# Kernel optimization log

Hardware: AMD Instinct MI355X
Metric: run time of the kernel (lower is better)

## Reference

```python
import jax, jax.numpy as jnp
import numpy as np

DECAY = 0.99
EPS = 1e-10
COMMIT = 0.25
K = 1024
D = 64


def setup_inputs() -> dict:
    key = jax.random.key(0)
    k1, k2, k3, k4 = jax.random.split(key, 4)
    return {
        "z_e": jax.random.normal(k1, (64, 64, 32, 32), dtype=jnp.float32),
        "embedding_w": jax.random.normal(k2, (K, D), dtype=jnp.float32),
        "ema_cluster_size": jax.random.uniform(k3, (K,), dtype=jnp.float32),
        "ema_w": jax.random.normal(k4, (K, D), dtype=jnp.float32),
    }


def reference(z_e, embedding_w, ema_cluster_size, ema_w):
    # [B, C, H, W] -> [B, H, W, C] -> [N, D]
    z_nhwc = jnp.transpose(z_e, (0, 2, 3, 1))
    z_flat = z_nhwc.reshape(-1, z_nhwc.shape[-1])

    # Squared-euclidean distances via ||z||^2 + ||e||^2 - 2 z e^T  -> [N, K]
    z_sq = jnp.sum(z_flat * z_flat, axis=1, keepdims=True)
    e_sq = jnp.sum(embedding_w * embedding_w, axis=1)
    distances = z_sq + e_sq - 2.0 * (z_flat @ embedding_w.T)

    indices = jnp.argmin(distances, axis=1)                      # [N]
    encodings = jax.nn.one_hot(indices, K, dtype=z_flat.dtype)   # [N, K]

    quantized = embedding_w[indices].reshape(z_nhwc.shape)       # [B, H, W, C]

    # --- EMA codebook update (training path; no-grad in original) ---
    counts = jnp.sum(encodings, axis=0)                          # [K]
    new_cluster_size = DECAY * ema_cluster_size + (1.0 - DECAY) * counts
    dw = encodings.T @ z_flat                                    # [K, D]
    new_ema_w = DECAY * ema_w + (1.0 - DECAY) * dw
    n = jnp.sum(new_cluster_size)
    cluster_size = (new_cluster_size + EPS) / (n + K * EPS) * n
    new_embedding_w = new_ema_w / cluster_size[:, None]

    # Commitment loss (quantized detached)
    diff = jax.lax.stop_gradient(quantized) - z_nhwc
    loss = COMMIT * jnp.mean(diff * diff)

    # Straight-through estimator
    quantized_st = z_nhwc + jax.lax.stop_gradient(quantized - z_nhwc)

    avg_probs = jnp.mean(encodings, axis=0)
    perplexity = jnp.exp(-jnp.sum(avg_probs * jnp.log(avg_probs + 1e-10)))

    quantized_out = jnp.transpose(quantized_st, (0, 3, 1, 2))    # [B, C, H, W]
    return (quantized_out, loss, perplexity, encodings,
            new_embedding_w, new_cluster_size, new_ema_w)
```

## Files before the change

### kernel.cpp

```cpp
#include <hip/hip_runtime.h>
#include <math.h>

#define NTOT 65536
#define KCB  1024
#define DIM  64

typedef float fvec2 __attribute__((ext_vector_type(2)));
typedef float fvec4 __attribute__((ext_vector_type(4)));
typedef short sh8  __attribute__((ext_vector_type(8)));

static const size_t OFF_Q    = 0;
static const size_t OFF_LOSS = 4194304;
static const size_t OFF_PERP = 4194305;
static const size_t OFF_ENC  = 4194306;
static const size_t OFF_EMB  = 71303170;
static const size_t OFF_NCS  = 71368706;
static const size_t OFF_NEMA = 71369730;

static const size_t WSO_IDX   = 0;
static const size_t WSO_ESQ   = 262144;
static const size_t WSO_LOSSP = 266240;
static const size_t WSO_CNT   = 270336;
static const size_t WSO_SCAL  = 274432;
static const size_t WSO_EBH   = 278528;
static const size_t WSO_EBL   = 409600;
static const size_t WSO_ZC    = 540672;
static const size_t WS_NEED_ZC = 540672 + (size_t)NTOT * DIM * 4;

__device__ __forceinline__ unsigned short f2bf(float f) {
    unsigned u = __builtin_bit_cast(unsigned, f);
    return (unsigned short)((u + 0x7FFFu + ((u >> 16) & 1u)) >> 16);
}
__device__ __forceinline__ float bf2f(unsigned short h) {
    unsigned u = ((unsigned)h) << 16;
    return __builtin_bit_cast(float, u);
}

__global__ void k_eprep(const float* __restrict__ emb,
                        unsigned short* __restrict__ ebh,
                        unsigned short* __restrict__ ebl,
                        float* __restrict__ esq) {
    int gid = blockIdx.x * 256 + threadIdx.x;
    int c = gid >> 3, ko8 = gid & 7;
    const fvec4* p = (const fvec4*)(emb + ((size_t)c << 6) + (ko8 << 3));
    fvec4 v0 = p[0], v1 = p[1];
    float f[8] = {v0.x, v0.y, v0.z, v0.w, v1.x, v1.y, v1.z, v1.w};
    sh8 h, l;
    float sq0 = 0.f, sq1 = 0.f;
#pragma unroll
    for (int j = 0; j < 8; ++j) {
        unsigned short hb = f2bf(f[j]);
        h[j] = (short)hb;
        l[j] = (short)f2bf(f[j] - bf2f(hb));
        if (j < 4) sq0 = fmaf(f[j], f[j], sq0); else sq1 = fmaf(f[j], f[j], sq1);
    }
    float sq = sq0 + sq1;
    sq += __shfl_xor(sq, 1, 64);
    sq += __shfl_xor(sq, 2, 64);
    sq += __shfl_xor(sq, 4, 64);
    if (ko8 == 0) esq[c] = sq;

    int ct = c >> 4, cl = c & 15, kc = ko8 >> 2, ko = ko8 & 3;
    size_t base = ((((size_t)ct << 1) + kc) << 9) + (((size_t)(ko << 4) + cl) << 3);
    *(sh8*)(ebh + base) = h;
    *(sh8*)(ebl + base) = l;
}

__global__ __launch_bounds__(256, 4)
void k_assign(const float* __restrict__ ze, const float* __restrict__ emb,
              const float* __restrict__ esq,
              const unsigned short* __restrict__ ebh,
              const unsigned short* __restrict__ ebl,
              int* __restrict__ idx_out, float* __restrict__ lossp,
              float* __restrict__ zc, int use_zc) {
    __shared__ float zt[4096];
    __shared__ float etq[4096];
    __shared__ int   sfidx[64];

    const int tid  = threadIdx.x;
    const int blk  = blockIdx.x;
    const int b    = blk >> 4;
    const int hw0  = (blk & 15) << 6;
    const int n0   = blk << 6;
    const int lane = tid & 63;
    const int wave = tid >> 6;
    const int cg   = lane & 15;
    const int ko   = lane >> 4;

#pragma unroll
    for (int j = 0; j < 4; ++j) {
        int idx = tid + (j << 8);
        int d = idx >> 4, r0 = (idx & 15) << 2;
        const fvec4 v = *(const fvec4*)(ze + (((size_t)(b << 6) + d) << 10) + hw0 + r0);
        zt[(r0 + 0) * 64 + d] = v.x;
        zt[(r0 + 1) * 64 + d] = v.y;
        zt[(r0 + 2) * 64 + d] = v.z;
        zt[(r0 + 3) * 64 + d] = v.w;
    }
    __syncthreads();

    const int arow = (wave << 4) + cg;
    sh8 Ah0, Ah1, Al0, Al1;
#pragma unroll
    for (int j = 0; j < 8; ++j) {
        float f0 = zt[arow * 64 + (ko << 3) + j];
        float f1 = zt[arow * 64 + 32 + (ko << 3) + j];
        unsigned short h0 = f2bf(f0), h1 = f2bf(f1);
        Ah0[j] = (short)h0;  Al0[j] = (short)f2bf(f0 - bf2f(h0));
        Ah1[j] = (short)h1;  Al1[j] = (short)f2bf(f1 - bf2f(h1));
    }

    float tb[4]  = {3.4e38f, 3.4e38f, 3.4e38f, 3.4e38f};
    float ts2[4] = {3.4e38f, 3.4e38f, 3.4e38f, 3.4e38f};
    int ti1[4] = {0, 0, 0, 0};
    int ti2[4] = {0, 0, 0, 0};

    const size_t lb = (size_t)lane << 3;
#define LOADB(d0, d1, d2, d3, ctv)                                  \
    { size_t o_ = ((size_t)(ctv) << 10) + lb;                       \
      d0 = *(const sh8*)(ebh + o_);                                 \
      d1 = *(const sh8*)(ebh + o_ + 512);                           \
      d2 = *(const sh8*)(ebl + o_);                                 \
      d3 = *(const sh8*)(ebl + o_ + 512); }

#define FOLD(ctv, acc)                                              \
    { const int code_ = ((ctv) << 4) + cg;                          \
      const float es_ = esq[code_];                                 \
      _Pragma("unroll")                                             \
      for (int rg = 0; rg < 4; ++rg) {                              \
          float s_ = fmaf((acc)[rg], -2.0f, es_);                   \
          bool c1 = s_ < tb[rg];                                    \
          bool c2 = s_ < ts2[rg];                                   \
          ti2[rg] = c1 ? ti1[rg] : (c2 ? code_ : ti2[rg]);          \
          ts2[rg] = c1 ? tb[rg] : (c2 ? s_ : ts2[rg]);              \
          ti1[rg] = c1 ? code_ : ti1[rg];                           \
          tb[rg]  = c1 ? s_ : tb[rg];                               \
      } }

#define TILE(i) ((((i) + (blk << 1)) & 63))

    sh8 b0h0, b0h1, b0l0, b0l1, b1h0, b1h1, b1l0, b1l1;
    LOADB(b0h0, b0h1, b0l0, b0l1, TILE(0));
    LOADB(b1h0, b1h1, b1l0, b1l1, TILE(1));

    for (int i = 0; i < 64; i += 2) {
        fvec4 aa = {0.f, 0.f, 0.f, 0.f}, ab = {0.f, 0.f, 0.f, 0.f};
        aa = __builtin_amdgcn_mfma_f32_16x16x32_bf16(Ah0, b0h0, aa, 0, 0, 0);
        ab = __builtin_amdgcn_mfma_f32_16x16x32_bf16(Ah1, b0h1, ab, 0, 0, 0);
        aa = __builtin_amdgcn_mfma_f32_16x16x32_bf16(Ah0, b0l0, aa, 0, 0, 0);
        ab = __builtin_amdgcn_mfma_f32_16x16x32_bf16(Ah1, b0l1, ab, 0, 0, 0);
        aa = __builtin_amdgcn_mfma_f32_16x16x32_bf16(Al0, b0h0, aa, 0, 0, 0);
        ab = __builtin_amdgcn_mfma_f32_16x16x32_bf16(Al1, b0h1, ab, 0, 0, 0);
        const int ct0 = TILE(i);
        if (i + 2 < 64) LOADB(b0h0, b0h1, b0l0, b0l1, TILE(i + 2));
        fvec4 acc0 = aa + ab;
        FOLD(ct0, acc0);

        fvec4 ba = {0.f, 0.f, 0.f, 0.f}, bb = {0.f, 0.f, 0.f, 0.f};
        ba = __builtin_amdgcn_mfma_f32_16x16x32_bf16(Ah0, b1h0, ba, 0, 0, 0);
        bb = __builtin_amdgcn_mfma_f32_16x16x32_bf16(Ah1, b1h1, bb, 0, 0, 0);
        ba = __builtin_amdgcn_mfma_f32_16x16x32_bf16(Ah0, b1l0, ba, 0, 0, 0);
        bb = __builtin_amdgcn_mfma_f32_16x16x32_bf16(Ah1, b1l1, bb, 0, 0, 0);
        ba = __builtin_amdgcn_mfma_f32_16x16x32_bf16(Al0, b1h0, ba, 0, 0, 0);
        bb = __builtin_amdgcn_mfma_f32_16x16x32_bf16(Al1, b1h1, bb, 0, 0, 0);
        const int ct1 = TILE(i + 1);
        if (i + 3 < 64) LOADB(b1h0, b1h1, b1l0, b1l1, TILE(i + 3));
        fvec4 acc1 = ba + bb;
        FOLD(ct1, acc1);
    }
#undef TILE
#undef LOADB
#undef FOLD

    float* mb  = etq;
    float* ms2 = etq + 1024;
    int*   mi1 = (int*)(etq + 2048);
    int*   mi2 = (int*)(etq + 3072);
#pragma unroll
    for (int rg = 0; rg < 4; ++rg) {
        int row = (wave << 4) + (ko << 2) + rg;
        mb [(cg << 6) + row] = tb[rg];
        ms2[(cg << 6) + row] = ts2[rg];
        mi1[(cg << 6) + row] = ti1[rg];
        mi2[(cg << 6) + row] = ti2[rg];
    }
    __syncthreads();

    if (tid < 64) {
        const int r = tid;
        float fb = mb[r], fs2 = ms2[r];
        int fi1 = mi1[r], fi2 = mi2[r];
#pragma unroll
        for (int p = 1; p < 16; ++p) {
            float ob = mb[(p << 6) + r], os2 = ms2[(p << 6) + r];
            int oi1 = mi1[(p << 6) + r], oi2 = mi2[(p << 6) + r];
            if (ob < fb)       { fs2 = fb; fi2 = fi1; fb = ob; fi1 = oi1; }
            else if (ob < fs2) { fs2 = ob; fi2 = oi1; }
            if (os2 < fs2)     { fs2 = os2; fi2 = oi2; }
        }
        if (fs2 - fb < 2e-2f) {
            double d1 = 0.0, d2 = 0.0;
            const float* e1 = emb + (size_t)fi1 * 64;
            const float* e2 = emb + (size_t)fi2 * 64;
            for (int d = 0; d < 64; ++d) {
                double zd = (double)zt[r * 64 + d];
                double q1 = zd - (double)e1[d];
                double q2 = zd - (double)e2[d];
                d1 += q1 * q1;
                d2 += q2 * q2;
            }
            if ((d2 < d1) || (d2 == d1 && fi2 < fi1)) fi1 = fi2;
        }
        sfidx[r] = fi1;
        idx_out[n0 + r] = fi1;
    }
    __syncthreads();

    float lacc = 0.f;
    for (int i = tid; i < 1024; i += 256) {
        int r = i >> 4, d4 = (i & 15) << 2;
        const fvec4 zv = *(const fvec4*)&zt[(r << 6) + d4];
        const fvec4 ev = *(const fvec4*)(emb + ((size_t)sfidx[r] << 6) + d4);
        fvec4 df = ev - zv;
        lacc = fmaf(df.x, df.x, lacc);
        lacc = fmaf(df.y, df.y, lacc);
        lacc = fmaf(df.z, df.z, lacc);
        lacc = fmaf(df.w, df.w, lacc);
        if (use_zc)
            *(fvec4*)&zc[(((size_t)(n0 + r)) << 6) + d4] = zv;
    }
    __syncthreads();

    float* lred = etq;
    lred[tid] = lacc;
    __syncthreads();
    for (int s = 128; s > 0; s >>= 1) {
        if (tid < s) lred[tid] += lred[tid + s];
        __syncthreads();
    }
    if (tid == 0) lossp[blk] = lred[0];
}

__global__ __launch_bounds__(256)
void k_tail(const int* __restrict__ idx, const float* __restrict__ zcmp,
            const float* __restrict__ ze, const float* __restrict__ emaw,
            const float* __restrict__ ecs, const float* __restrict__ emb,
            float* __restrict__ out, int* __restrict__ counts, int use_zc) {
    __shared__ __align__(16) char smem[17424];
    const int t = threadIdx.x;

    if (blockIdx.x & 1) {
        const int blk = blockIdx.x >> 1;
        const int b   = blk >> 4;
        const int hw0 = (blk & 15) << 6;
        const int n0  = blk << 6;
        int*   sfidx = (int*)smem;
        float* qt    = (float*)(smem + 256);

        if (t < 64) sfidx[t] = idx[n0 + t];
        __syncthreads();

        for (int i = t; i < 4096; i += 256) {
            int r = i >> 6, d = i & 63;
            qt[d * 65 + r] = emb[(size_t)sfidx[r] * 64 + d];
        }

        float* ebase = out + OFF_ENC;
        if (t < 255) {
            const int cb = 2 + (t << 2);
            for (int r = 0; r < 64; ++r) {
                const int fi = sfidx[r];
                fvec4 v;
                v.x = (fi == cb)     ? 1.0f : 0.0f;
                v.y = (fi == cb + 1) ? 1.0f : 0.0f;
                v.z = (fi == cb + 2) ? 1.0f : 0.0f;
                v.w = (fi == cb + 3) ? 1.0f : 0.0f;
                __builtin_nontemporal_store(
                    v, (fvec4*)(ebase + ((size_t)(n0 + r) << 10) + cb));
            }
        } else {
            for (int r = 0; r < 64; ++r) {
                const int fi = sfidx[r];
                float* rowp = ebase + ((size_t)(n0 + r) << 10);
                fvec2 hd, tl;
                hd.x = (fi == 0)    ? 1.0f : 0.0f;
                hd.y = (fi == 1)    ? 1.0f : 0.0f;
                tl.x = (fi == 1022) ? 1.0f : 0.0f;
                tl.y = (fi == 1023) ? 1.0f : 0.0f;
                __builtin_nontemporal_store(hd, (fvec2*)rowp);
                __builtin_nontemporal_store(tl, (fvec2*)(rowp + 1022));
            }
        }
        __syncthreads();

        for (int i = t; i < 4096; i += 256) {
            int d = i >> 6, r = i & 63;
            __builtin_nontemporal_store(
                qt[d * 65 + r],
                &out[OFF_Q + ((size_t)((b << 6) + d) << 10) + hw0 + r]);
        }
        return;
    }

    const int k    = blockIdx.x >> 1;
    const int g    = t >> 6;
    const int d    = t & 63;
    const int lane = t & 63;
    int*   s_list = (int*)smem;
    int*   s_wsum = (int*)(smem + 16384);
    float* s_red  = (float*)(smem + 16400);

#define ZLOAD(n) (use_zc ? zcmp[((size_t)(n) << 6) + d] \
                         : ze[((((size_t)((n) >> 10) << 6) + d) << 10) + ((n) & 1023)])

    float a0 = 0.f, a1 = 0.f, a2 = 0.f, a3 = 0.f;
    int totalM = 0;

    for (int chunk = 0; chunk < 16; ++chunk) {
        const int base = chunk << 12;
        const int nb   = base + (t << 4);
        const int4* ip = (const int4*)(idx + nb);
        const int4 v0 = ip[0], v1 = ip[1], v2 = ip[2], v3 = ip[3];

        int c = 0;
        c += (v0.x == k) + (v0.y == k) + (v0.z == k) + (v0.w == k);
        c += (v1.x == k) + (v1.y == k) + (v1.z == k) + (v1.w == k);
        c += (v2.x == k) + (v2.y == k) + (v2.z == k) + (v2.w == k);
        c += (v3.x == k) + (v3.y == k) + (v3.z == k) + (v3.w == k);

        int inc = c;
#pragma unroll
        for (int off = 1; off < 64; off <<= 1) {
            int y = __shfl_up(inc, (unsigned)off, 64);
            if (lane >= off) inc += y;
        }
        if (lane == 63) s_wsum[g] = inc;
        __syncthreads();

        int wbase = 0;
#pragma unroll
        for (int w = 0; w < 4; ++w) wbase += (w < g) ? s_wsum[w] : 0;
        const int M = s_wsum[0] + s_wsum[1] + s_wsum[2] + s_wsum[3];
        int pos = wbase + inc - c;

        if (v0.x == k) s_list[pos++] = nb + 0;
        if (v0.y == k) s_list[pos++] = nb + 1;
        if (v0.z == k) s_list[pos++] = nb + 2;
        if (v0.w == k) s_list[pos++] = nb + 3;
        if (v1.x == k) s_list[pos++] = nb + 4;
        if (v1.y == k) s_list[pos++] = nb + 5;
        if (v1.z == k) s_list[pos++] = nb + 6;
        if (v1.w == k) s_list[pos++] = nb + 7;
        if (v2.x == k) s_list[pos++] = nb + 8;
        if (v2.y == k) s_list[pos++] = nb + 9;
        if (v2.z == k) s_list[pos++] = nb + 10;
        if (v2.w == k) s_list[pos++] = nb + 11;
        if (v3.x == k) s_list[pos++] = nb + 12;
        if (v3.y == k) s_list[pos++] = nb + 13;
        if (v3.z == k) s_list[pos++] = nb + 14;
        if (v3.w == k) s_list[pos++] = nb + 15;
        __syncthreads();

        int j = g;
        for (; j + 12 < M; j += 16) {
            int n0_ = s_list[j], n1_ = s_list[j + 4];
            int n2_ = s_list[j + 8], n3_ = s_list[j + 12];
            float z0 = ZLOAD(n0_), z1 = ZLOAD(n1_);
            float z2 = ZLOAD(n2_), z3 = ZLOAD(n3_);
            a0 += z0; a1 += z1; a2 += z2; a3 += z3;
        }
        for (; j < M; j += 4) a0 += ZLOAD(s_list[j]);
        totalM += M;
        __syncthreads();
    }
#undef ZLOAD

    s_red[(g << 6) + d] = (a0 + a1) + (a2 + a3);
    __syncthreads();
    if (g == 0) {
        float s = ((s_red[d] + s_red[64 + d]) + s_red[128 + d]) + s_red[192 + d];
        out[OFF_NEMA + ((size_t)k << 6) + d] =
            fmaf(0.01f, s, 0.99f * emaw[((size_t)k << 6) + d]);
    }
    if (t == 0) {
        counts[k] = totalM;
        out[OFF_NCS + k] = fmaf(0.01f, (float)totalM, 0.99f * ecs[k]);
    }
}

__global__ void k_scalars(const float* __restrict__ lossp, const int* __restrict__ counts,
                          const float* __restrict__ ncs, float* __restrict__ out,
                          float* __restrict__ scal) {
    __shared__ float sr[256];
    const int t = threadIdx.x;

    float v = lossp[t] + lossp[t + 256] + lossp[t + 512] + lossp[t + 768];
    sr[t] = v;
    __syncthreads();
    for (int s = 128; s > 0; s >>= 1) { if (t < s) sr[t] += sr[t + s]; __syncthreads(); }
    if (t == 0) out[OFF_LOSS] = sr[0] * (0.25f / 4194304.0f);
    __syncthreads();

    v = ncs[t] + ncs[t + 256] + ncs[t + 512] + ncs[t + 768];
    sr[t] = v;
    __syncthreads();
    for (int s = 128; s > 0; s >>= 1) { if (t < s) sr[t] += sr[t + s]; __syncthreads(); }
    if (t == 0) scal[0] = sr[0];
    __syncthreads();

    float pv = 0.f;
    for (int i = t; i < 1024; i += 256) {
        float p = (float)counts[i] * (1.0f / 65536.0f);
        pv += p * logf(p + 1e-10f);
    }
    sr[t] = pv;
    __syncthreads();
    for (int s = 128; s > 0; s >>= 1) { if (t < s) sr[t] += sr[t + s]; __syncthreads(); }
    if (t == 0) out[OFF_PERP] = expf(-sr[0]);
}

__global__ void k_embnorm(const float* __restrict__ nema, const float* __restrict__ ncs,
                          const float* __restrict__ scal, float* __restrict__ embw) {
    int i = blockIdx.x * 256 + threadIdx.x;
    float n = scal[0];
    int k = i >> 6;
    float cs = (ncs[k] + 1e-10f) / (n + 1.024e-7f) * n;
    embw[i] = nema[i] / cs;
}

extern "C" void kernel_launch(void* const* d_in, const int* in_sizes, int n_in,
                              void* d_out, int out_size, void* d_ws, size_t ws_size,
                              hipStream_t stream) {
    const float* ze   = (const float*)d_in[0];
    const float* emb  = (const float*)d_in[1];
    const float* ecs  = (const float*)d_in[2];
    const float* emaw = (const float*)d_in[3];
    float* out = (float*)d_out;
    char*  ws  = (char*)d_ws;

    int*            idx    = (int*)(ws + WSO_IDX);
    float*          esq    = (float*)(ws + WSO_ESQ);
    float*          lossp  = (float*)(ws + WSO_LOSSP);
    int*            counts = (int*)(ws + WSO_CNT);
    float*          scal   = (float*)(ws + WSO_SCAL);
    unsigned short* ebh    = (unsigned short*)(ws + WSO_EBH);
    unsigned short* ebl    = (unsigned short*)(ws + WSO_EBL);
    float*          zc     = (float*)(ws + WSO_ZC);
    const int use_zc = (ws_size >= WS_NEED_ZC) ? 1 : 0;

    k_eprep  <<<32,   256, 0, stream>>>(emb, ebh, ebl, esq);
    k_assign <<<1024, 256, 0, stream>>>(ze, emb, esq, ebh, ebl, idx, lossp, zc, use_zc);
    k_tail   <<<2048, 256, 0, stream>>>(idx, zc, ze, emaw, ecs, emb, out, counts, use_zc);
    k_scalars<<<1,    256, 0, stream>>>(lossp, counts, out + OFF_NCS, out, scal);
    k_embnorm<<<256,  256, 0, stream>>>(out + OFF_NEMA, out + OFF_NCS, scal, out + OFF_EMB);
}
```

Measured before the change: 153.2 us.

## Stage codebook tiles through a double-buffered LDS ring shared by the block

Previously each of the four waves loaded every bf16 hi/lo codebook tile straight from global memory into registers, so each tile was fetched four times per block. Now the block loads each tile cooperatively, one 16-byte load per thread, and stores it into a two-slot LDS buffer; every wave then reads its MFMA operands from LDS. The esq norms are also copied into LDS once per block. The cost is a __syncthreads per tile, 64 per block, and shorter per-wave prefetch distance, which can stall the small 6-MFMA loop body.

After: 164.6 us. +7.4%, slower.

```diff
diff --git a/kernel.cpp b/kernel.cpp
--- a/kernel.cpp
+++ b/kernel.cpp
@@ -74,7 +74,7 @@
               int* __restrict__ idx_out, float* __restrict__ lossp,
               float* __restrict__ zc, int use_zc) {
     __shared__ float zt[4096];
-    __shared__ float etq[4096];
+    __shared__ __align__(16) float etq[4096];
     __shared__ int   sfidx[64];
 
     const int tid  = threadIdx.x;
@@ -87,6 +87,10 @@
     const int cg   = lane & 15;
     const int ko   = lane >> 4;
 
+    char*  ebuf0 = (char*)etq;
+    char*  ebuf1 = (char*)etq + 4096;
+    float* esql  = etq + 2048;
+
 #pragma unroll
     for (int j = 0; j < 4; ++j) {
         int idx = tid + (j << 8);
@@ -97,6 +101,19 @@
         zt[(r0 + 2) * 64 + d] = v.z;
         zt[(r0 + 3) * 64 + d] = v.w;
     }
+    {
+        fvec4 e4 = *(const fvec4*)(esq + (tid << 2));
+        *(fvec4*)&esql[tid << 2] = e4;
+    }
+
+    const unsigned short* sgbase = (tid < 128) ? ebh : ebl;
+    const int soff   = (tid & 127) << 3;
+    const int dstoff = (tid < 128) ? (tid << 4) : (2048 + ((tid - 128) << 4));
+    const size_t lo  = (size_t)lane << 4;
+
+#define TILE(i) ((((i) + (blk << 1)) & 63))
+
+    sh8 stg = *(const sh8*)(sgbase + ((size_t)TILE(0) << 10) + soff);
     __syncthreads();
 
     const int arow = (wave << 4) + cg;
@@ -110,67 +127,52 @@
         Ah1[j] = (short)h1;  Al1[j] = (short)f2bf(f1 - bf2f(h1));
     }
 
+    *(sh8*)(ebuf0 + dstoff) = stg;
+    __syncthreads();
+
     float tb[4]  = {3.4e38f, 3.4e38f, 3.4e38f, 3.4e38f};
     float ts2[4] = {3.4e38f, 3.4e38f, 3.4e38f, 3.4e38f};
     int ti1[4] = {0, 0, 0, 0};
     int ti2[4] = {0, 0, 0, 0};
 
-    const size_t lb = (size_t)lane << 3;
-#define LOADB(d0, d1, d2, d3, ctv)                                  \
-    { size_t o_ = ((size_t)(ctv) << 10) + lb;                       \
-      d0 = *(const sh8*)(ebh + o_);                                 \
-      d1 = *(const sh8*)(ebh + o_ + 512);                           \
-      d2 = *(const sh8*)(ebl + o_);                                 \
-      d3 = *(const sh8*)(ebl + o_ + 512); }
-
-#define FOLD(ctv, acc)                                              \
-    { const int code_ = ((ctv) << 4) + cg;                          \
-      const float es_ = esq[code_];                                 \
-      _Pragma("unroll")                                             \
-      for (int rg = 0; rg < 4; ++rg) {                              \
-          float s_ = fmaf((acc)[rg], -2.0f, es_);                   \
-          bool c1 = s_ < tb[rg];                                    \
-          bool c2 = s_ < ts2[rg];                                   \
-          ti2[rg] = c1 ? ti1[rg] : (c2 ? code_ : ti2[rg]);          \
-          ts2[rg] = c1 ? tb[rg] : (c2 ? s_ : ts2[rg]);              \
-          ti1[rg] = c1 ? code_ : ti1[rg];                           \
-          tb[rg]  = c1 ? s_ : tb[rg];                               \
-      } }
-
-#define TILE(i) ((((i) + (blk << 1)) & 63))
-
-    sh8 b0h0, b0h1, b0l0, b0l1, b1h0, b1h1, b1l0, b1l1;
-    LOADB(b0h0, b0h1, b0l0, b0l1, TILE(0));
-    LOADB(b1h0, b1h1, b1l0, b1l1, TILE(1));
-
-    for (int i = 0; i < 64; i += 2) {
+    for (int i = 0; i < 64; ++i) {
+        const int ct = TILE(i);
+        const char* rb = (i & 1) ? ebuf1 : ebuf0;
+        char*       wb = (i & 1) ? ebuf0 : ebuf1;
+        if (i < 63)
+            stg = *(const sh8*)(sgbase + ((size_t)TILE(i + 1) << 10) + soff);
+
+        sh8 bh0 = *(const sh8*)(rb + lo);
+        sh8 bh1 = *(const sh8*)(rb + 1024 + lo);
+        sh8 bl0 = *(const sh8*)(rb + 2048 + lo);
+        sh8 bl1 = *(const sh8*)(rb + 3072 + lo);
+
         fvec4 aa = {0.f, 0.f, 0.f, 0.f}, ab = {0.f, 0.f, 0.f, 0.f};
-        aa = __builtin_amdgcn_mfma_f32_16x16x32_bf16(Ah0, b0h0, aa, 0, 0, 0);
-        ab = __builtin_amdgcn_mfma_f32_16x16x32_bf16(Ah1, b0h1, ab, 0, 0, 0);
-        aa = __builtin_amdgcn_mfma_f32_16x16x32_bf16(Ah0, b0l0, aa, 0, 0, 0);
-        ab = __builtin_amdgcn_mfma_f32_16x16x32_bf16(Ah1, b0l1, ab, 0, 0, 0);
-        aa = __builtin_amdgcn_mfma_f32_16x16x32_bf16(Al0, b0h0, aa, 0, 0, 0);
-        ab = __builtin_amdgcn_mfma_f32_16x16x32_bf16(Al1, b0h1, ab, 0, 0, 0);
-        const int ct0 = TILE(i);
-        if (i + 2 < 64) LOADB(b0h0, b0h1, b0l0, b0l1, TILE(i + 2));
-        fvec4 acc0 = aa + ab;
-        FOLD(ct0, acc0);
-
-        fvec4 ba = {0.f, 0.f, 0.f, 0.f}, bb = {0.f, 0.f, 0.f, 0.f};
-        ba = __builtin_amdgcn_mfma_f32_16x16x32_bf16(Ah0, b1h0, ba, 0, 0, 0);
-        bb = __builtin_amdgcn_mfma_f32_16x16x32_bf16(Ah1, b1h1, bb, 0, 0, 0);
-        ba = __builtin_amdgcn_mfma_f32_16x16x32_bf16(Ah0, b1l0, ba, 0, 0, 0);
-        bb = __builtin_amdgcn_mfma_f32_16x16x32_bf16(Ah1, b1l1, bb, 0, 0, 0);
-        ba = __builtin_amdgcn_mfma_f32_16x16x32_bf16(Al0, b1h0, ba, 0, 0, 0);
-        bb = __builtin_amdgcn_mfma_f32_16x16x32_bf16(Al1, b1h1, bb, 0, 0, 0);
-        const int ct1 = TILE(i + 1);
-        if (i + 3 < 64) LOADB(b1h0, b1h1, b1l0, b1l1, TILE(i + 3));
-        fvec4 acc1 = ba + bb;
-        FOLD(ct1, acc1);
+        aa = __builtin_amdgcn_mfma_f32_16x16x32_bf16(Ah0, bh0, aa, 0, 0, 0);
+        ab = __builtin_amdgcn_mfma_f32_16x16x32_bf16(Ah1, bh1, ab, 0, 0, 0);
+        aa = __builtin_amdgcn_mfma_f32_16x16x32_bf16(Ah0, bl0, aa, 0, 0, 0);
+        ab = __builtin_amdgcn_mfma_f32_16x16x32_bf16(Ah1, bl1, ab, 0, 0, 0);
+        aa = __builtin_amdgcn_mfma_f32_16x16x32_bf16(Al0, bh0, aa, 0, 0, 0);
+        ab = __builtin_amdgcn_mfma_f32_16x16x32_bf16(Al1, bh1, ab, 0, 0, 0);
+        fvec4 acc = aa + ab;
+
+        const int code = (ct << 4) + cg;
+        const float es = esql[code];
+#pragma unroll
+        for (int rg = 0; rg < 4; ++rg) {
+            float s = fmaf(acc[rg], -2.0f, es);
+            bool c1 = s < tb[rg];
+            bool c2 = s < ts2[rg];
+            ti2[rg] = c1 ? ti1[rg] : (c2 ? code : ti2[rg]);
+            ts2[rg] = c1 ? tb[rg] : (c2 ? s : ts2[rg]);
+            ti1[rg] = c1 ? code : ti1[rg];
+            tb[rg]  = c1 ? s : tb[rg];
+        }
+
+        if (i < 63) *(sh8*)(wb + dstoff) = stg;
+        __syncthreads();
     }
 #undef TILE
-#undef LOADB
-#undef FOLD
 
     float* mb  = etq;
     float* ms2 = etq + 1024;
```

## Fuse one-hot and quantized output writes into assign kernel; prefetch esq

Applied to the files above, without the earlier changes.

Moves the one-hot encoding stores and the transposed quantized-output writes from the tail kernel into the assignment kernel. The gathered codebook rows already in registers are staged through a swizzled shared-memory tile, which avoids re-reading indices and embeddings in a separate pass. The tail kernel becomes a stats-only kernel with half the blocks. It also software-prefetches the esq value alongside the B-tile loads. The trade-off is a longer assign kernel, so the large 268MB encoding write is no longer overlapped with the stats blocks in the same launch.

New measurement: 187.4 us. 1.22x slower.

```diff
diff --git a/kernel.cpp b/kernel.cpp
--- a/kernel.cpp
+++ b/kernel.cpp
@@ -34,6 +34,10 @@
 __device__ __forceinline__ float bf2f(unsigned short h) {
     unsigned u = ((unsigned)h) << 16;
     return __builtin_bit_cast(float, u);
+}
+
+__device__ __forceinline__ int swz(int r, int d) {
+    return (r << 6) + ((((d >> 2) ^ ((r >> 2) & 15)) << 2) | (d & 3));
 }
 
 __global__ void k_eprep(const float* __restrict__ emb,
@@ -71,10 +75,11 @@
               const float* __restrict__ esq,
               const unsigned short* __restrict__ ebh,
               const unsigned short* __restrict__ ebl,
+              float* __restrict__ out,
               int* __restrict__ idx_out, float* __restrict__ lossp,
               float* __restrict__ zc, int use_zc) {
     __shared__ float zt[4096];
-    __shared__ float etq[4096];
+    __shared__ __align__(16) float etq[4096];
     __shared__ int   sfidx[64];
 
     const int tid  = threadIdx.x;
@@ -123,12 +128,11 @@
       d2 = *(const sh8*)(ebl + o_);                                 \
       d3 = *(const sh8*)(ebl + o_ + 512); }
 
-#define FOLD(ctv, acc)                                              \
+#define FOLD(ctv, acc, esv)                                         \
     { const int code_ = ((ctv) << 4) + cg;                          \
-      const float es_ = esq[code_];                                 \
       _Pragma("unroll")                                             \
       for (int rg = 0; rg < 4; ++rg) {                              \
-          float s_ = fmaf((acc)[rg], -2.0f, es_);                   \
+          float s_ = fmaf((acc)[rg], -2.0f, (esv));                 \
           bool c1 = s_ < tb[rg];                                    \
           bool c2 = s_ < ts2[rg];                                   \
           ti2[rg] = c1 ? ti1[rg] : (c2 ? code_ : ti2[rg]);          \
@@ -142,6 +146,8 @@
     sh8 b0h0, b0h1, b0l0, b0l1, b1h0, b1h1, b1l0, b1l1;
     LOADB(b0h0, b0h1, b0l0, b0l1, TILE(0));
     LOADB(b1h0, b1h1, b1l0, b1l1, TILE(1));
+    float es0 = esq[(TILE(0) << 4) + cg];
+    float es1 = esq[(TILE(1) << 4) + cg];
 
     for (int i = 0; i < 64; i += 2) {
         fvec4 aa = {0.f, 0.f, 0.f, 0.f}, ab = {0.f, 0.f, 0.f, 0.f};
@@ -152,9 +158,13 @@
         aa = __builtin_amdgcn_mfma_f32_16x16x32_bf16(Al0, b0h0, aa, 0, 0, 0);
         ab = __builtin_amdgcn_mfma_f32_16x16x32_bf16(Al1, b0h1, ab, 0, 0, 0);
         const int ct0 = TILE(i);
-        if (i + 2 < 64) LOADB(b0h0, b0h1, b0l0, b0l1, TILE(i + 2));
+        const float esc0 = es0;
+        if (i + 2 < 64) {
+            LOADB(b0h0, b0h1, b0l0, b0l1, TILE(i + 2));
+            es0 = esq[(TILE(i + 2) << 4) + cg];
+        }
         fvec4 acc0 = aa + ab;
-        FOLD(ct0, acc0);
+        FOLD(ct0, acc0, esc0);
 
         fvec4 ba = {0.f, 0.f, 0.f, 0.f}, bb = {0.f, 0.f, 0.f, 0.f};
         ba = __builtin_amdgcn_mfma_f32_16x16x32_bf16(Ah0, b1h0, ba, 0, 0, 0);
@@ -164,9 +174,13 @@
         ba = __builtin_amdgcn_mfma_f32_16x16x32_bf16(Al0, b1h0, ba, 0, 0, 0);
         bb = __builtin_amdgcn_mfma_f32_16x16x32_bf16(Al1, b1h1, bb, 0, 0, 0);
         const int ct1 = TILE(i + 1);
-        if (i + 3 < 64) LOADB(b1h0, b1h1, b1l0, b1l1, TILE(i + 3));
+        const float esc1 = es1;
+        if (i + 3 < 64) {
+            LOADB(b1h0, b1h1, b1l0, b1l1, TILE(i + 3));
+            es1 = esq[(TILE(i + 3) << 4) + cg];
+        }
         fvec4 acc1 = ba + bb;
-        FOLD(ct1, acc1);
+        FOLD(ct1, acc1, esc1);
     }
 #undef TILE
 #undef LOADB
@@ -226,8 +240,47 @@
         lacc = fmaf(df.y, df.y, lacc);
         lacc = fmaf(df.z, df.z, lacc);
         lacc = fmaf(df.w, df.w, lacc);
+        etq[swz(d4 + 0, r)] = ev.x;
+        etq[swz(d4 + 1, r)] = ev.y;
+        etq[swz(d4 + 2, r)] = ev.z;
+        etq[swz(d4 + 3, r)] = ev.w;
         if (use_zc)
             *(fvec4*)&zc[(((size_t)(n0 + r)) << 6) + d4] = zv;
+    }
+
+    float* ebase = out + OFF_ENC;
+    if (tid < 255) {
+        const int cb = 2 + (tid << 2);
+        for (int r = 0; r < 64; ++r) {
+            const int fi = sfidx[r];
+            fvec4 v;
+            v.x = (fi == cb)     ? 1.0f : 0.0f;
+            v.y = (fi == cb + 1) ? 1.0f : 0.0f;
+            v.z = (fi == cb + 2) ? 1.0f : 0.0f;
+            v.w = (fi == cb + 3) ? 1.0f : 0.0f;
+            __builtin_nontemporal_store(
+                v, (fvec4*)(ebase + ((size_t)(n0 + r) << 10) + cb));
+        }
+    } else {
+        for (int r = 0; r < 64; ++r) {
+            const int fi = sfidx[r];
+            float* rowp = ebase + ((size_t)(n0 + r) << 10);
+            fvec2 hd, tl;
+            hd.x = (fi == 0)    ? 1.0f : 0.0f;
+            hd.y = (fi == 1)    ? 1.0f : 0.0f;
+            tl.x = (fi == 1022) ? 1.0f : 0.0f;
+            tl.y = (fi == 1023) ? 1.0f : 0.0f;
+            __builtin_nontemporal_store(hd, (fvec2*)rowp);
+            __builtin_nontemporal_store(tl, (fvec2*)(rowp + 1022));
+        }
+    }
+    __syncthreads();
+
+    for (int i = tid; i < 4096; i += 256) {
+        int d = i >> 6, r = i & 63;
+        __builtin_nontemporal_store(
+            etq[swz(d, r)],
+            &out[OFF_Q + ((size_t)((b << 6) + d) << 10) + hw0 + r]);
     }
     __syncthreads();
 
@@ -242,73 +295,19 @@
 }
 
 __global__ __launch_bounds__(256)
-void k_tail(const int* __restrict__ idx, const float* __restrict__ zcmp,
-            const float* __restrict__ ze, const float* __restrict__ emaw,
-            const float* __restrict__ ecs, const float* __restrict__ emb,
-            float* __restrict__ out, int* __restrict__ counts, int use_zc) {
-    __shared__ __align__(16) char smem[17424];
-    const int t = threadIdx.x;
-
-    if (blockIdx.x & 1) {
-        const int blk = blockIdx.x >> 1;
-        const int b   = blk >> 4;
-        const int hw0 = (blk & 15) << 6;
-        const int n0  = blk << 6;
-        int*   sfidx = (int*)smem;
-        float* qt    = (float*)(smem + 256);
-
-        if (t < 64) sfidx[t] = idx[n0 + t];
-        __syncthreads();
-
-        for (int i = t; i < 4096; i += 256) {
-            int r = i >> 6, d = i & 63;
-            qt[d * 65 + r] = emb[(size_t)sfidx[r] * 64 + d];
-        }
-
-        float* ebase = out + OFF_ENC;
-        if (t < 255) {
-            const int cb = 2 + (t << 2);
-            for (int r = 0; r < 64; ++r) {
-                const int fi = sfidx[r];
-                fvec4 v;
-                v.x = (fi == cb)     ? 1.0f : 0.0f;
-                v.y = (fi == cb + 1) ? 1.0f : 0.0f;
-                v.z = (fi == cb + 2) ? 1.0f : 0.0f;
-                v.w = (fi == cb + 3) ? 1.0f : 0.0f;
-                __builtin_nontemporal_store(
-                    v, (fvec4*)(ebase + ((size_t)(n0 + r) << 10) + cb));
-            }
-        } else {
-            for (int r = 0; r < 64; ++r) {
-                const int fi = sfidx[r];
-                float* rowp = ebase + ((size_t)(n0 + r) << 10);
-                fvec2 hd, tl;
-                hd.x = (fi == 0)    ? 1.0f : 0.0f;
-                hd.y = (fi == 1)    ? 1.0f : 0.0f;
-                tl.x = (fi == 1022) ? 1.0f : 0.0f;
-                tl.y = (fi == 1023) ? 1.0f : 0.0f;
-                __builtin_nontemporal_store(hd, (fvec2*)rowp);
-                __builtin_nontemporal_store(tl, (fvec2*)(rowp + 1022));
-            }
-        }
-        __syncthreads();
-
-        for (int i = t; i < 4096; i += 256) {
-            int d = i >> 6, r = i & 63;
-            __builtin_nontemporal_store(
-                qt[d * 65 + r],
-                &out[OFF_Q + ((size_t)((b << 6) + d) << 10) + hw0 + r]);
-        }
-        return;
-    }
-
-    const int k    = blockIdx.x >> 1;
+void k_stats(const int* __restrict__ idx, const float* __restrict__ zcmp,
+             const float* __restrict__ ze, const float* __restrict__ emaw,
+             const float* __restrict__ ecs, float* __restrict__ out,
+             int* __restrict__ counts, int use_zc) {
+    const int k    = blockIdx.x;
+    const int t    = threadIdx.x;
     const int g    = t >> 6;
     const int d    = t & 63;
     const int lane = t & 63;
-    int*   s_list = (int*)smem;
-    int*   s_wsum = (int*)(smem + 16384);
-    float* s_red  = (float*)(smem + 16400);
+
+    __shared__ int   s_list[4096];
+    __shared__ int   s_wsum[4];
+    __shared__ float s_red[4][64];
 
 #define ZLOAD(n) (use_zc ? zcmp[((size_t)(n) << 6) + d] \
                          : ze[((((size_t)((n) >> 10) << 6) + d) << 10) + ((n) & 1023)])
@@ -375,10 +374,10 @@
     }
 #undef ZLOAD
 
-    s_red[(g << 6) + d] = (a0 + a1) + (a2 + a3);
+    s_red[g][d] = (a0 + a1) + (a2 + a3);
     __syncthreads();
     if (g == 0) {
-        float s = ((s_red[d] + s_red[64 + d]) + s_red[128 + d]) + s_red[192 + d];
+        float s = ((s_red[0][d] + s_red[1][d]) + s_red[2][d]) + s_red[3][d];
         out[OFF_NEMA + ((size_t)k << 6) + d] =
             fmaf(0.01f, s, 0.99f * emaw[((size_t)k << 6) + d]);
     }
@@ -449,8 +448,8 @@
     const int use_zc = (ws_size >= WS_NEED_ZC) ? 1 : 0;
 
     k_eprep  <<<32,   256, 0, stream>>>(emb, ebh, ebl, esq);
-    k_assign <<<1024, 256, 0, stream>>>(ze, emb, esq, ebh, ebl, idx, lossp, zc, use_zc);
-    k_tail   <<<2048, 256, 0, stream>>>(idx, zc, ze, emaw, ecs, emb, out, counts, use_zc);
+    k_assign <<<1024, 256, 0, stream>>>(ze, emb, esq, ebh, ebl, out, idx, lossp, zc, use_zc);
+    k_stats  <<<1024, 256, 0, stream>>>(idx, zc, ze, emaw, ecs, out, counts, use_zc);
     k_scalars<<<1,    256, 0, stream>>>(lossp, counts, out + OFF_NCS, out, scal);
     k_embnorm<<<256,  256, 0, stream>>>(out + OFF_NEMA, out + OFF_NCS, scal, out + OFF_EMB);
 }
```

## Split codebook scatter into 16-code by 4096-row tiles with separate reduction kernel

Applied to the files above, without the earlier changes.

Before, each k_tail block owned one code and scanned all 65536 indices across 16 chunks. Now each block owns 16 codes and a 4096-row slice. It accumulates per-code partial sums in shared memory, tallies counts with LDS atomics, and writes partials to workspace. A new k_red kernel sums the 16 slices and applies the EMA update. The aim is to cut the redundant index scanning by 16x, at the cost of an extra launch, about 4MB of partial traffic, and a larger shared-memory footprint per block.

Measured after the change: 155.1 us. No clear change (+1.3%).

```diff
diff --git a/kernel.cpp b/kernel.cpp
--- a/kernel.cpp
+++ b/kernel.cpp
@@ -24,8 +24,10 @@
 static const size_t WSO_SCAL  = 274432;
 static const size_t WSO_EBH   = 278528;
 static const size_t WSO_EBL   = 409600;
-static const size_t WSO_ZC    = 540672;
-static const size_t WS_NEED_ZC = 540672 + (size_t)NTOT * DIM * 4;
+static const size_t WSO_PDW   = 540672;
+static const size_t WSO_PCNT  = 4734976;
+static const size_t WSO_ZC    = 4800512;
+static const size_t WS_NEED_ZC = 4800512 + (size_t)NTOT * DIM * 4;
 
 __device__ __forceinline__ unsigned short f2bf(float f) {
     unsigned u = __builtin_bit_cast(unsigned, f);
@@ -243,10 +245,10 @@
 
 __global__ __launch_bounds__(256)
 void k_tail(const int* __restrict__ idx, const float* __restrict__ zcmp,
-            const float* __restrict__ ze, const float* __restrict__ emaw,
-            const float* __restrict__ ecs, const float* __restrict__ emb,
-            float* __restrict__ out, int* __restrict__ counts, int use_zc) {
-    __shared__ __align__(16) char smem[17424];
+            const float* __restrict__ ze, const float* __restrict__ emb,
+            float* __restrict__ out, float* __restrict__ pdw,
+            int* __restrict__ pcnt, int use_zc) {
+    __shared__ __align__(16) char smem[32864];
     const int t = threadIdx.x;
 
     if (blockIdx.x & 1) {
@@ -302,89 +304,104 @@
         return;
     }
 
-    const int k    = blockIdx.x >> 1;
+    const int sidx = blockIdx.x >> 1;
+    const int kg   = sidx & 63;
+    const int ng   = sidx >> 6;
+    const int k0   = kg << 4;
     const int g    = t >> 6;
     const int d    = t & 63;
     const int lane = t & 63;
+
     int*   s_list = (int*)smem;
-    int*   s_wsum = (int*)(smem + 16384);
-    float* s_red  = (float*)(smem + 16400);
-
-#define ZLOAD(n) (use_zc ? zcmp[((size_t)(n) << 6) + d] \
-                         : ze[((((size_t)((n) >> 10) << 6) + d) << 10) + ((n) & 1023)])
-
-    float a0 = 0.f, a1 = 0.f, a2 = 0.f, a3 = 0.f;
-    int totalM = 0;
-
-    for (int chunk = 0; chunk < 16; ++chunk) {
-        const int base = chunk << 12;
-        const int nb   = base + (t << 4);
-        const int4* ip = (const int4*)(idx + nb);
-        const int4 v0 = ip[0], v1 = ip[1], v2 = ip[2], v3 = ip[3];
-
+    float* part   = (float*)(smem + 16384);
+    int*   s_wsum = (int*)(smem + 32768);
+    int*   s_cnt  = (int*)(smem + 32784);
+
+    for (int i = t; i < 4096; i += 256) part[i] = 0.f;
+    if (t < 16) s_cnt[t] = 0;
+
+    const int nb = (ng << 12) + (t << 4);
+    const int4* ip = (const int4*)(idx + nb);
+    const int4 v0 = ip[0], v1 = ip[1], v2 = ip[2], v3 = ip[3];
+
+#define MM(x) ((unsigned)((x) - k0) < 16u)
+    int c = 0;
+    c += MM(v0.x) + MM(v0.y) + MM(v0.z) + MM(v0.w);
+    c += MM(v1.x) + MM(v1.y) + MM(v1.z) + MM(v1.w);
+    c += MM(v2.x) + MM(v2.y) + MM(v2.z) + MM(v2.w);
+    c += MM(v3.x) + MM(v3.y) + MM(v3.z) + MM(v3.w);
+
+    int inc = c;
+#pragma unroll
+    for (int off = 1; off < 64; off <<= 1) {
+        int y = __shfl_up(inc, (unsigned)off, 64);
+        if (lane >= off) inc += y;
+    }
+    if (lane == 63) s_wsum[g] = inc;
+    __syncthreads();
+
+    int wbase = 0;
+#pragma unroll
+    for (int w = 0; w < 4; ++w) wbase += (w < g) ? s_wsum[w] : 0;
+    const int M = s_wsum[0] + s_wsum[1] + s_wsum[2] + s_wsum[3];
+    int pos = wbase + inc - c;
+
+#define EMIT(x, o) if (MM(x)) { s_list[pos++] = (((t << 4) + (o)) << 4) | ((x) - k0); \
+                                atomicAdd(&s_cnt[(x) - k0], 1); }
+    EMIT(v0.x, 0)  EMIT(v0.y, 1)  EMIT(v0.z, 2)  EMIT(v0.w, 3)
+    EMIT(v1.x, 4)  EMIT(v1.y, 5)  EMIT(v1.z, 6)  EMIT(v1.w, 7)
+    EMIT(v2.x, 8)  EMIT(v2.y, 9)  EMIT(v2.z, 10) EMIT(v2.w, 11)
+    EMIT(v3.x, 12) EMIT(v3.y, 13) EMIT(v3.z, 14) EMIT(v3.w, 15)
+#undef EMIT
+#undef MM
+    __syncthreads();
+
+#define ZL(nloc) (use_zc ? zcmp[(((size_t)((ng << 12) + (nloc))) << 6) + d] \
+                         : ze[((((size_t)(((ng << 12) + (nloc)) >> 10) << 6) + d) << 10) + (((ng << 12) + (nloc)) & 1023)])
+    {
+        float* pg = part + (g << 10);
+        int j = g;
+        for (; j + 4 < M; j += 8) {
+            int e0 = s_list[j], e1 = s_list[j + 4];
+            float f0 = ZL(e0 >> 4);
+            float f1 = ZL(e1 >> 4);
+            pg[((e0 & 15) << 6) + d] += f0;
+            pg[((e1 & 15) << 6) + d] += f1;
+        }
+        for (; j < M; j += 4) {
+            int e0 = s_list[j];
+            pg[((e0 & 15) << 6) + d] += ZL(e0 >> 4);
+        }
+    }
+#undef ZL
+    __syncthreads();
+
+    for (int i = t; i < 1024; i += 256) {
+        float s = ((part[i] + part[1024 + i]) + part[2048 + i]) + part[3072 + i];
+        int cc = i >> 6, dd = i & 63;
+        pdw[(((size_t)(ng << 10) + k0 + cc) << 6) + dd] = s;
+    }
+    if (t < 16) pcnt[(ng << 10) + k0 + t] = s_cnt[t];
+}
+
+__global__ __launch_bounds__(256)
+void k_red(const float* __restrict__ pdw, const int* __restrict__ pcnt,
+           const float* __restrict__ emaw, const float* __restrict__ ecs,
+           float* __restrict__ out, int* __restrict__ counts) {
+    const int gid = blockIdx.x * 256 + threadIdx.x;
+    const int k = gid >> 6, d = gid & 63;
+    float s = 0.f;
+#pragma unroll
+    for (int ng = 0; ng < 16; ++ng)
+        s += pdw[(((size_t)(ng << 10) + k) << 6) + d];
+    out[OFF_NEMA + ((size_t)k << 6) + d] =
+        fmaf(0.01f, s, 0.99f * emaw[((size_t)k << 6) + d]);
+    if (d == 0) {
         int c = 0;
-        c += (v0.x == k) + (v0.y == k) + (v0.z == k) + (v0.w == k);
-        c += (v1.x == k) + (v1.y == k) + (v1.z == k) + (v1.w == k);
-        c += (v2.x == k) + (v2.y == k) + (v2.z == k) + (v2.w == k);
-        c += (v3.x == k) + (v3.y == k) + (v3.z == k) + (v3.w == k);
-
-        int inc = c;
-#pragma unroll
-        for (int off = 1; off < 64; off <<= 1) {
-            int y = __shfl_up(inc, (unsigned)off, 64);
-            if (lane >= off) inc += y;
-        }
-        if (lane == 63) s_wsum[g] = inc;
-        __syncthreads();
-
-        int wbase = 0;
-#pragma unroll
-        for (int w = 0; w < 4; ++w) wbase += (w < g) ? s_wsum[w] : 0;
-        const int M = s_wsum[0] + s_wsum[1] + s_wsum[2] + s_wsum[3];
-        int pos = wbase + inc - c;
-
-        if (v0.x == k) s_list[pos++] = nb + 0;
-        if (v0.y == k) s_list[pos++] = nb + 1;
-        if (v0.z == k) s_list[pos++] = nb + 2;
-        if (v0.w == k) s_list[pos++] = nb + 3;
-        if (v1.x == k) s_list[pos++] = nb + 4;
-        if (v1.y == k) s_list[pos++] = nb + 5;
-        if (v1.z == k) s_list[pos++] = nb + 6;
-        if (v1.w == k) s_list[pos++] = nb + 7;
-        if (v2.x == k) s_list[pos++] = nb + 8;
-        if (v2.y == k) s_list[pos++] = nb + 9;
-        if (v2.z == k) s_list[pos++] = nb + 10;
-        if (v2.w == k) s_list[pos++] = nb + 11;
-        if (v3.x == k) s_list[pos++] = nb + 12;
-        if (v3.y == k) s_list[pos++] = nb + 13;
-        if (v3.z == k) s_list[pos++] = nb + 14;
-        if (v3.w == k) s_list[pos++] = nb + 15;
-        __syncthreads();
-
-        int j = g;
-        for (; j + 12 < M; j += 16) {
-            int n0_ = s_list[j], n1_ = s_list[j + 4];
-            int n2_ = s_list[j + 8], n3_ = s_list[j + 12];
-            float z0 = ZLOAD(n0_), z1 = ZLOAD(n1_);
-            float z2 = ZLOAD(n2_), z3 = ZLOAD(n3_);
-            a0 += z0; a1 += z1; a2 += z2; a3 += z3;
-        }
-        for (; j < M; j += 4) a0 += ZLOAD(s_list[j]);
-        totalM += M;
-        __syncthreads();
-    }
-#undef ZLOAD
-
-    s_red[(g << 6) + d] = (a0 + a1) + (a2 + a3);
-    __syncthreads();
-    if (g == 0) {
-        float s = ((s_red[d] + s_red[64 + d]) + s_red[128 + d]) + s_red[192 + d];
-        out[OFF_NEMA + ((size_t)k << 6) + d] =
-            fmaf(0.01f, s, 0.99f * emaw[((size_t)k << 6) + d]);
-    }
-    if (t == 0) {
-        counts[k] = totalM;
-        out[OFF_NCS + k] = fmaf(0.01f, (float)totalM, 0.99f * ecs[k]);
+#pragma unroll
+        for (int ng = 0; ng < 16; ++ng) c += pcnt[(ng << 10) + k];
+        counts[k] = c;
+        out[OFF_NCS + k] = fmaf(0.01f, (float)c, 0.99f * ecs[k]);
     }
 }
 
@@ -445,12 +462,15 @@
     float*          scal   = (float*)(ws + WSO_SCAL);
     unsigned short* ebh    = (unsigned short*)(ws + WSO_EBH);
     unsigned short* ebl    = (unsigned short*)(ws + WSO_EBL);
+    float*          pdw    = (float*)(ws + WSO_PDW);
+    int*            pcnt   = (int*)(ws + WSO_PCNT);
     float*          zc     = (float*)(ws + WSO_ZC);
     const int use_zc = (ws_size >= WS_NEED_ZC) ? 1 : 0;
 
     k_eprep  <<<32,   256, 0, stream>>>(emb, ebh, ebl, esq);
     k_assign <<<1024, 256, 0, stream>>>(ze, emb, esq, ebh, ebl, idx, lossp, zc, use_zc);
-    k_tail   <<<2048, 256, 0, stream>>>(idx, zc, ze, emaw, ecs, emb, out, counts, use_zc);
+    k_tail   <<<2048, 256, 0, stream>>>(idx, zc, ze, emb, out, pdw, pcnt, use_zc);
+    k_red    <<<256,  256, 0, stream>>>(pdw, pcnt, emaw, ecs, out, counts);
     k_scalars<<<1,    256, 0, stream>>>(lossp, counts, out + OFF_NCS, out, scal);
     k_embnorm<<<256,  256, 0, stream>>>(out + OFF_NEMA, out + OFF_NCS, scal, out + OFF_EMB);
 }
```
